# Optimization experiments

Measured on AMD Instinct MI355X. Metric: run time of the kernel, lower is better.

The kernel has to match this reference:

```python
import jax, jax.numpy as jnp
import numpy as np

NUM_HEADS = 32
NUM_KV_HEADS = 8
HEAD_DIM = 128
HIDDEN = 4096
BASE = 10000.0


def setup_inputs() -> dict:
    key = jax.random.key(0)
    ks = jax.random.split(key, 9)
    bs, seq = 1, 2048
    x = jax.random.normal(ks[0], (bs, seq, HIDDEN), dtype=jnp.float32)
    position_ids = jnp.broadcast_to(jnp.arange(seq, dtype=jnp.int32), (bs, seq))
    s = 1.0 / np.sqrt(HIDDEN)
    wq = jax.random.normal(ks[1], (NUM_HEADS * HEAD_DIM, HIDDEN), dtype=jnp.float32) * s
    bq = jnp.zeros((NUM_HEADS * HEAD_DIM,), dtype=jnp.float32)
    wk = jax.random.normal(ks[2], (NUM_KV_HEADS * HEAD_DIM, HIDDEN), dtype=jnp.float32) * s
    bk = jnp.zeros((NUM_KV_HEADS * HEAD_DIM,), dtype=jnp.float32)
    wv = jax.random.normal(ks[3], (NUM_KV_HEADS * HEAD_DIM, HIDDEN), dtype=jnp.float32) * s
    bv = jnp.zeros((NUM_KV_HEADS * HEAD_DIM,), dtype=jnp.float32)
    wo = jax.random.normal(ks[4], (HIDDEN, NUM_HEADS * HEAD_DIM), dtype=jnp.float32) * s
    bo = jnp.zeros((HIDDEN,), dtype=jnp.float32)
    return {"x": x, "position_ids": position_ids, "wq": wq, "bq": bq,
            "wk": wk, "bk": bk, "wv": wv, "bv": bv, "wo": wo, "bo": bo}


def _rotate_half(t):
    h = t.shape[-1] // 2
    return jnp.concatenate([-t[..., h:], t[..., :h]], axis=-1)


def _rope_cos_sin(position_ids, dtype):
    # inv_freq: (head_dim/2,)
    inv_freq = 1.0 / (BASE ** (jnp.arange(0, HEAD_DIM, 2, dtype=jnp.float32) / HEAD_DIM))
    freqs = position_ids.astype(jnp.float32)[..., None] * inv_freq  # (bs, seq, hd/2)
    emb = jnp.concatenate([freqs, freqs], axis=-1)  # (bs, seq, hd)
    return jnp.cos(emb).astype(dtype), jnp.sin(emb).astype(dtype)


def reference(x, position_ids, wq, bq, wk, bk, wv, bv, wo, bo):
    bs, seq, _ = x.shape
    g = NUM_HEADS // NUM_KV_HEADS
    # projections -> (bs, heads, seq, head_dim)
    q = (x @ wq.T + bq).reshape(bs, seq, NUM_HEADS, HEAD_DIM).transpose(0, 2, 1, 3)
    k = (x @ wk.T + bk).reshape(bs, seq, NUM_KV_HEADS, HEAD_DIM).transpose(0, 2, 1, 3)
    v = (x @ wv.T + bv).reshape(bs, seq, NUM_KV_HEADS, HEAD_DIM).transpose(0, 2, 1, 3)
    cos, sin = _rope_cos_sin(position_ids, x.dtype)
    cos, sin = cos[:, None], sin[:, None]  # broadcast over heads
    q = q * cos + _rotate_half(q) * sin
    k = k * cos + _rotate_half(k) * sin
    # grouped attention without expanding kv (same math as repeat_kv)
    qg = q.reshape(bs, NUM_KV_HEADS, g, seq, HEAD_DIM)
    scores = jnp.einsum('bhgqd,bhkd->bhgqk', qg, k) / jnp.sqrt(
        jnp.asarray(HEAD_DIM, dtype=jnp.float32)).astype(x.dtype)
    probs = jax.nn.softmax(scores.astype(jnp.float32), axis=-1).astype(x.dtype)
    out = jnp.einsum('bhgqk,bhkd->bhgqd', probs, v)  # (bs, kvh, g, seq, hd)
    out = out.reshape(bs, NUM_HEADS, seq, HEAD_DIM).transpose(0, 2, 1, 3)
    out = out.reshape(bs, seq, NUM_HEADS * HEAD_DIM)
    return out @ wo.T + bo
```

## Files before the change

kernel.cpp:

```cpp
#include <hip/hip_runtime.h>
#include <stdint.h>

typedef unsigned short u16;
typedef unsigned long long u64;
typedef __attribute__((ext_vector_type(8))) short s8v;
typedef __attribute__((ext_vector_type(4))) float f4v;

#define MFMA(a, b, c) __builtin_amdgcn_mfma_f32_16x16x32_bf16((a), (b), (c), 0, 0, 0)

__device__ __forceinline__ u16 f2b(float f) {
  uint32_t x = __float_as_uint(f);
  x += 0x7fff + ((x >> 16) & 1);
  return (u16)(x >> 16);
}
__device__ __forceinline__ float b2f(u16 u) {
  return __uint_as_float(((uint32_t)u) << 16);
}

__device__ __forceinline__ void gll16(const void* g, void* l) {
  __builtin_amdgcn_global_load_lds((const __attribute__((address_space(1))) uint32_t*)g,
                                   (__attribute__((address_space(3))) uint32_t*)l, 16, 0, 0);
}
__device__ __forceinline__ void bar() { __builtin_amdgcn_s_barrier(); }

__global__ void cvt_kernel(const float* __restrict__ src, u16* __restrict__ dst, int n8) {
  int i = blockIdx.x * 256 + threadIdx.x;
  if (i >= n8) return;
  const float4* s = (const float4*)src;
  float4 f0 = s[2 * (size_t)i], f1 = s[2 * (size_t)i + 1];
  s8v o;
  o[0] = (short)f2b(f0.x); o[1] = (short)f2b(f0.y); o[2] = (short)f2b(f0.z); o[3] = (short)f2b(f0.w);
  o[4] = (short)f2b(f1.x); o[5] = (short)f2b(f1.y); o[6] = (short)f2b(f1.z); o[7] = (short)f2b(f1.w);
  *(s8v*)(dst + 8 * (size_t)i) = o;
}

template <int BM, int MODE>
__global__ __launch_bounds__(512, 2) void gemm8p(
    const u16* __restrict__ A, const u16* __restrict__ Bact,
    const float* __restrict__ bA, const float* __restrict__ bB, const float* __restrict__ bC,
    float* __restrict__ Cf, u16* __restrict__ Cq, u16* __restrict__ Ck, u16* __restrict__ Cv,
    int K) {
  extern __shared__ u16 smem[];
  constexpr int AO = BM * 64;
  constexpr int BE = 2 * BM * 64;
  constexpr int BO = BE + 16384;
  constexpr int MI = BM / 64;

  const int tid = threadIdx.x;
  const int l = tid & 63, wv = tid >> 6;
  const int wm = wv >> 2, wn = wv & 3;
  const int lr = l & 15, lg = l >> 4;
  const int swz = 16 * (lr & 7);
  const int wrow = wm * (BM / 2);

  const int nwg = gridDim.x;
  int bid = blockIdx.x;
  bid = (bid & 7) * (nwg >> 3) + (bid >> 3);
  const int NB = 8;
  const int m0 = (bid / NB) * BM, n0 = (bid % NB) * 256;

  const size_t K64 = (size_t)64 * K;

  const int sr = tid >> 3;
  const int sc = ((tid & 7) ^ (sr & 7)) * 8;
  const u16* gA = A + (size_t)(m0 + sr) * K + sc;
  const u16* gB = Bact + (size_t)(n0 + sr) * K + sc;

  auto STA = [&](int P, int h, int kt) {
    const u16* g = gA + (size_t)(h * (BM / 2)) * K + (size_t)kt * 64;
    u16* d = smem + (P ? AO : 0) + h * (BM / 2) * 64 + tid * 8;
    gll16(g, d);
    if constexpr (BM == 256) gll16(g + K64, d + 4096);
  };
  auto STB = [&](int P, int h, int kt) {
    const u16* g = gB + (size_t)(h * 128) * K + (size_t)kt * 64;
    u16* d = smem + (P ? BO : BE) + h * 8192 + tid * 8;
    gll16(g, d);
    gll16(g + K64, d + 4096);
  };

  const char* smc = (const char*)smem;
  s8v a[MI][2], b0[2][2], b1[2][2];
  auto LDA = [&](int P, int QR) {
#pragma unroll
    for (int mi = 0; mi < MI; ++mi)
#pragma unroll
      for (int kk = 0; kk < 2; ++kk)
        a[mi][kk] = *(const s8v*)(smc + (P ? AO * 2 : 0) +
            (wrow + QR * (BM / 4) + mi * 16 + lr) * 128 + ((kk * 64 + lg * 16) ^ swz));
  };
  auto LDB = [&](int P, int QC, s8v bb[2][2]) {
#pragma unroll
    for (int ni = 0; ni < 2; ++ni)
#pragma unroll
      for (int kk = 0; kk < 2; ++kk)
        bb[ni][kk] = *(const s8v*)(smc + (P ? BO * 2 : BE * 2) +
            (wn * 64 + QC * 32 + ni * 16 + lr) * 128 + ((kk * 64 + lg * 16) ^ swz));
  };

  f4v acc[BM / 32][4];
#pragma unroll
  for (int i = 0; i < BM / 32; ++i)
#pragma unroll
    for (int j = 0; j < 4; ++j) acc[i][j] = {0.f, 0.f, 0.f, 0.f};

#define PHMF(QR, QC, B)                                                        \
  __builtin_amdgcn_s_setprio(1);                                               \
  _Pragma("unroll") for (int mi = 0; mi < MI; ++mi)                            \
    _Pragma("unroll") for (int ni = 0; ni < 2; ++ni)                           \
      _Pragma("unroll") for (int kk = 0; kk < 2; ++kk)                         \
        acc[(QR) * MI + mi][(QC) * 2 + ni] =                                   \
            MFMA(a[mi][kk], B[ni][kk], acc[(QR) * MI + mi][(QC) * 2 + ni]);    \
  __builtin_amdgcn_s_setprio(0);

  STB(0, 0, 0); STB(0, 1, 0);
  STA(0, 0, 0); STA(0, 1, 0);
  STB(1, 0, 1); STB(1, 1, 1);
  asm volatile("s_waitcnt vmcnt(4)" ::: "memory");
  bar();

  const int ITERS = K >> 7;
  for (int i = 0; i < ITERS; ++i) {
    const int kn = 2 * i + 2;
    const bool more = (i + 1 < ITERS);
    LDA(0, 0); LDB(0, 0, b0);
    STA(1, 0, 2 * i + 1);
    bar(); PHMF(0, 0, b0); bar();
    LDB(0, 1, b1);
    STA(1, 1, 2 * i + 1);
    bar(); PHMF(0, 1, b1); bar();
    LDA(0, 1);
    if (more) STB(0, 0, kn);
    bar(); PHMF(1, 1, b1); bar();
    if (more) STB(0, 1, kn);
    bar(); PHMF(1, 0, b0);
    asm volatile("s_waitcnt vmcnt(4)" ::: "memory");
    bar();
    LDA(1, 0); LDB(1, 0, b0);
    if (more) STA(0, 0, kn);
    bar(); PHMF(0, 0, b0); bar();
    LDB(1, 1, b1);
    if (more) STA(0, 1, kn);
    bar(); PHMF(0, 1, b1); bar();
    LDA(1, 1);
    if (more) STB(1, 0, 2 * i + 3);
    bar(); PHMF(1, 1, b1); bar();
    if (more) STB(1, 1, 2 * i + 3);
    bar(); PHMF(1, 0, b0);
    asm volatile("s_waitcnt vmcnt(4)" ::: "memory");
    bar();
  }
#undef PHMF

  bar();

  if (MODE == 2) {
    const int mt = m0 >> 8;
    if (mt < 20) {
      u16* dst; int fstride, fbase; const float* bias;
      if (mt < 16) { dst = Cq; fstride = 4096; fbase = m0;        bias = bA; }
      else         { dst = Ck; fstride = 1024; fbase = m0 - 4096; bias = bB; }
      u16* buf = smem + wv * 4352;
#pragma unroll
      for (int c = 0; c < 2; ++c) {
#pragma unroll
        for (int fj2 = 0; fj2 < 2; ++fj2) {
          const int fj = 2 * c + fj2;
          const int tl = fj2 * 16 + lr;
#pragma unroll
          for (int fi = 0; fi < BM / 32; ++fi)
#pragma unroll
            for (int r = 0; r < 4; ++r) {
              const int fl = fi * 16 + lg * 4 + r;
              buf[tl * 136 + fl] = f2b(acc[fi][fj][r] + bias[fbase + wrow + fl]);
            }
        }
        asm volatile("s_waitcnt lgkmcnt(0)" ::: "memory");
        const int row = l >> 1, half = l & 1;
        const int tok = n0 + wn * 64 + c * 32 + row;
        const u16* src = buf + row * 136 + half * 64;
        u16* g = dst + (size_t)tok * fstride + fbase + wrow + half * 64;
#pragma unroll
        for (int i = 0; i < 8; ++i)
          *(s8v*)(g + i * 8) = *(const s8v*)(src + i * 8);
        asm volatile("s_waitcnt lgkmcnt(0)" ::: "memory");
      }
    } else {
#pragma unroll
      for (int fi = 0; fi < BM / 32; ++fi)
#pragma unroll
        for (int fj = 0; fj < 4; ++fj)
#pragma unroll
          for (int r = 0; r < 4; ++r) {
            const int feat = m0 - 5120 + wrow + fi * 16 + lg * 4 + r;
            const int tok = n0 + wn * 64 + fj * 16 + lr;
            Cv[(size_t)feat * 2048 + tok] = f2b(acc[fi][fj][r] + bC[feat]);
          }
    }
  } else {
    float* buf = (float*)smem + wv * 1088;
#pragma unroll
    for (int c = 0; c < 4; ++c) {
#pragma unroll
      for (int fi = 0; fi < BM / 32; ++fi)
#pragma unroll
        for (int r = 0; r < 4; ++r) {
          const int fl = fi * 16 + lg * 4 + r;
          buf[lr * 68 + fl] = acc[fi][c][r] + bA[m0 + wrow + fl];
        }
      asm volatile("s_waitcnt lgkmcnt(0)" ::: "memory");
      const int row = l >> 2, q4 = l & 3;
      const int tok = n0 + wn * 64 + c * 16 + row;
      float* g = Cf + (size_t)tok * 4096 + m0 + wrow + q4 * 16;
      const float* src = buf + row * 68 + q4 * 16;
#pragma unroll
      for (int i = 0; i < 4; ++i)
        *(f4v*)(g + i * 4) = *(const f4v*)(src + i * 4);
      asm volatile("s_waitcnt lgkmcnt(0)" ::: "memory");
    }
  }
}

__global__ void rope_kernel(u16* __restrict__ q, u16* __restrict__ k, const int* __restrict__ pos) {
  int i = blockIdx.x * 256 + threadIdx.x;
  const int NQ = 2048 * 32 * 64;
  const int NK = 2048 * 8 * 64;
  u16* buf;
  int m, d, stride, h;
  if (i < NQ) { buf = q; m = i >> 11; h = (i >> 6) & 31; d = i & 63; stride = 4096; }
  else {
    i -= NQ; if (i >= NK) return;
    buf = k; m = i >> 9; h = (i >> 6) & 7; d = i & 63; stride = 1024;
  }
  size_t base = (size_t)m * stride + h * 128 + d;
  float a = b2f(buf[base]), b = b2f(buf[base + 64]);
  float p = (float)pos[m];
  float ang = p * exp2f(-0.20762050593045952f * (float)d);
  float s, c;
  sincosf(ang, &s, &c);
  buf[base]      = f2b(a * c - b * s);
  buf[base + 64] = f2b(b * c + a * s);
}

__global__ __launch_bounds__(512, 4) void attn_kernel(const u16* __restrict__ Q, const u16* __restrict__ Kb,
                                                      const u16* __restrict__ Vt, u16* __restrict__ Ao) {
  __shared__ __align__(16) u16 Ks[64 * 128];
  __shared__ __align__(16) u16 Vs[128 * 64];
  __shared__ __align__(16) u16 Ps[8 * 16 * 64];
  const int tid = threadIdx.x;
  const int l = tid & 63, wv = tid >> 6;
  const int lr = l & 15, lg = l >> 4;
  const int head = blockIdx.x >> 4, qt = blockIdx.x & 15;
  const int kh = head >> 2;
  const int qrow = qt * 128 + wv * 16 + lr;

  s8v qf[4];
#pragma unroll
  for (int s = 0; s < 4; ++s)
    qf[s] = *(const s8v*)&Q[(size_t)qrow * 4096 + head * 128 + s * 32 + lg * 8];

  f4v zero = {0.f, 0.f, 0.f, 0.f};
  f4v ao[8];
#pragma unroll
  for (int tt = 0; tt < 8; ++tt) ao[tt] = zero;
  float mrun = -1e30f, lrun = 0.f;

  const int ki0 = tid, ki1 = tid + 512;
  const int kr0 = ki0 >> 4, kc0 = (ki0 & 15) ^ (kr0 & 7);
  const int kr1 = ki1 >> 4, kc1 = (ki1 & 15) ^ (kr1 & 7);
  const int vr0 = ki0 >> 3, vc0 = (ki0 & 7) ^ (vr0 & 7);
  const int vr1 = ki1 >> 3, vc1 = (ki1 & 7) ^ (vr1 & 7);
  const u16* Kg = Kb + kh * 128;
  const u16* Vg = Vt + (size_t)(kh * 128) * 2048;
  const u16* kp0 = Kg + (size_t)kr0 * 1024 + kc0 * 8;
  const u16* kp1 = Kg + (size_t)kr1 * 1024 + kc1 * 8;
  const u16* vp0 = Vg + (size_t)vr0 * 2048 + vc0 * 8;
  const u16* vp1 = Vg + (size_t)vr1 * 2048 + vc1 * 8;

  char* KsB = (char*)Ks;
  char* VsB = (char*)Vs;
  char* PwB = (char*)Ps + wv * 2048;
  const int swz = 16 * (lr & 7);
  const float C2 = 0.12753102f;

  for (int t = 0; t < 2048; t += 64) {
    __syncthreads();
    gll16(kp0 + (size_t)t * 1024, KsB + ki0 * 16);
    gll16(kp1 + (size_t)t * 1024, KsB + ki1 * 16);
    gll16(vp0 + t,                VsB + ki0 * 16);
    gll16(vp1 + t,                VsB + ki1 * 16);
    __syncthreads();

    f4v c[4];
#pragma unroll
    for (int j = 0; j < 4; ++j) c[j] = zero;
#pragma unroll
    for (int s = 0; s < 4; ++s) {
#pragma unroll
      for (int j = 0; j < 4; ++j) {
        s8v kf = *(const s8v*)(KsB + (16 * j + lr) * 256 + (((4 * s + lg) * 16) ^ swz));
        c[j] = MFMA(kf, qf[s], c[j]);
      }
    }

    float mx = fmaxf(fmaxf(c[0][0], c[0][1]), fmaxf(c[0][2], c[0][3]));
#pragma unroll
    for (int j = 1; j < 4; ++j)
      mx = fmaxf(mx, fmaxf(fmaxf(c[j][0], c[j][1]), fmaxf(c[j][2], c[j][3])));
    mx = fmaxf(mx, __shfl_xor(mx, 16));
    mx = fmaxf(mx, __shfl_xor(mx, 32));
    float m2x = mx * C2;

    if (!__all(m2x - mrun <= 8.f)) {
      float mnew = fmaxf(mrun, m2x);
      float alpha = __builtin_amdgcn_exp2f(mrun - mnew);
      float ar[4];
#pragma unroll
      for (int r = 0; r < 4; ++r) ar[r] = __shfl(alpha, 4 * lg + r);
#pragma unroll
      for (int tt = 0; tt < 8; ++tt)
#pragma unroll
        for (int r = 0; r < 4; ++r) ao[tt][r] *= ar[r];
      lrun *= alpha;
      mrun = mnew;
    }

    float rs = 0.f;
#pragma unroll
    for (int j = 0; j < 4; ++j) {
      float p0 = __builtin_amdgcn_exp2f(__builtin_fmaf(c[j][0], C2, -mrun));
      float p1 = __builtin_amdgcn_exp2f(__builtin_fmaf(c[j][1], C2, -mrun));
      float p2 = __builtin_amdgcn_exp2f(__builtin_fmaf(c[j][2], C2, -mrun));
      float p3 = __builtin_amdgcn_exp2f(__builtin_fmaf(c[j][3], C2, -mrun));
      rs += (p0 + p1) + (p2 + p3);
      uint32_t lo = (uint32_t)f2b(p0) | ((uint32_t)f2b(p1) << 16);
      uint32_t hi = (uint32_t)f2b(p2) | ((uint32_t)f2b(p3) << 16);
      u64 pak = (u64)lo | ((u64)hi << 32);
      *(u64*)(PwB + lr * 128 + ((32 * j + 8 * lg) ^ swz)) = pak;
    }
    rs += __shfl_xor(rs, 16);
    rs += __shfl_xor(rs, 32);
    lrun += rs;

#pragma unroll
    for (int h = 0; h < 2; ++h) {
      s8v pf = *(const s8v*)(PwB + lr * 128 + ((64 * h + 16 * lg) ^ swz));
#pragma unroll
      for (int tt = 0; tt < 8; ++tt) {
        s8v vf = *(const s8v*)(VsB + (16 * tt + lr) * 128 + (((4 * h + lg) * 16) ^ swz));
        ao[tt] = MFMA(pf, vf, ao[tt]);
      }
    }
  }

  float inv = 1.f / lrun;
  float ir[4];
#pragma unroll
  for (int r = 0; r < 4; ++r) ir[r] = __shfl(inv, 4 * lg + r);
#pragma unroll
  for (int tt = 0; tt < 8; ++tt)
#pragma unroll
    for (int r = 0; r < 4; ++r)
      Ao[(size_t)(qt * 128 + wv * 16 + 4 * lg + r) * 4096 + head * 128 + 16 * tt + lr] =
          f2b(ao[tt][r] * ir[r]);
}

extern "C" void kernel_launch(void* const* d_in, const int* in_sizes, int n_in,
                              void* d_out, int out_size, void* d_ws, size_t ws_size,
                              hipStream_t stream) {
  const float* x  = (const float*)d_in[0];
  const int*   pos = (const int*)d_in[1];
  const float* wq = (const float*)d_in[2];
  const float* bq = (const float*)d_in[3];
  const float* wk = (const float*)d_in[4];
  const float* bk = (const float*)d_in[5];
  const float* wv = (const float*)d_in[6];
  const float* bv = (const float*)d_in[7];
  const float* wo = (const float*)d_in[8];
  const float* bo = (const float*)d_in[9];
  float* out = (float*)d_out;

  char* ws = (char*)d_ws;
  u16* xb   = (u16*)(ws + 0);
  u16* wqkv = (u16*)(ws + 16777216);
  u16* wob  = (u16*)(ws + 67108864);
  u16* qb   = (u16*)(ws + 100663296);
  u16* kb   = (u16*)(ws + 117440512);
  u16* vT   = (u16*)(ws + 121634816);
  u16* ab   = (u16*)(ws + 125829120);

  auto cv = [&](const float* s, u16* d, size_t n) {
    int n8 = (int)(n / 8);
    cvt_kernel<<<(n8 + 255) / 256, 256, 0, stream>>>(s, d, n8);
  };
  cv(x,  xb,   (size_t)2048 * 4096);
  cv(wq, wqkv, (size_t)4096 * 4096);
  cv(wk, wqkv + (size_t)4096 * 4096, (size_t)1024 * 4096);
  cv(wv, wqkv + (size_t)5120 * 4096, (size_t)1024 * 4096);
  cv(wo, wob,  (size_t)4096 * 4096);

  gemm8p<256, 2><<<192, 512, 131072, stream>>>(wqkv, xb, bq, bk, bv,
                                               nullptr, qb, kb, vT, 4096);
  rope_kernel<<<(2048 * 32 * 64 + 2048 * 8 * 64) / 256, 256, 0, stream>>>(qb, kb, pos);
  attn_kernel<<<512, 512, 0, stream>>>(qb, kb, vT, ab);
  gemm8p<128, 0><<<256, 512, 98304, stream>>>(wob, ab, bo, nullptr, nullptr,
                                              out, nullptr, nullptr, nullptr, 4096);
}
```

Before: 347.0 us.

## Use 192-row QKV GEMM tiles, merge conversion kernels, concatenate biases

Changes the fused QKV projection GEMM from 256-row to 192-row tiles so 6144 rows give 256 workgroups instead of 192, which fits the CU count better. The A-tile staging loop and the epilogue are generalized so one tile can straddle the Q/K/V boundaries, with a per-fragment split between direct V writes and LDS-staged Q/K writes. The five fp32-to-bf16 conversion launches are merged into one kernel, and the biases are copied into one contiguous buffer with three async device copies. The cost is more complex epilogue branching and extra small memcpy launches.

```diff
diff --git a/kernel.cpp b/kernel.cpp
--- a/kernel.cpp
+++ b/kernel.cpp
@@ -23,21 +23,29 @@
 }
 __device__ __forceinline__ void bar() { __builtin_amdgcn_s_barrier(); }
 
-__global__ void cvt_kernel(const float* __restrict__ src, u16* __restrict__ dst, int n8) {
+__global__ void cvt_all(const float* __restrict__ x, const float* __restrict__ wq,
+                        const float* __restrict__ wk, const float* __restrict__ wv,
+                        const float* __restrict__ wo,
+                        u16* __restrict__ xb, u16* __restrict__ wqkv, u16* __restrict__ wob) {
   int i = blockIdx.x * 256 + threadIdx.x;
-  if (i >= n8) return;
-  const float4* s = (const float4*)src;
-  float4 f0 = s[2 * (size_t)i], f1 = s[2 * (size_t)i + 1];
+  const float* s; u16* d; size_t off;
+  if      (i < 1048576) { s = x;  d = xb;   off = (size_t)i; }
+  else if (i < 3145728) { s = wq; d = wqkv; off = (size_t)(i - 1048576); }
+  else if (i < 3670016) { s = wk; d = wqkv + (size_t)16777216; off = (size_t)(i - 3145728); }
+  else if (i < 4194304) { s = wv; d = wqkv + (size_t)20971520; off = (size_t)(i - 3670016); }
+  else                  { s = wo; d = wob;  off = (size_t)(i - 4194304); }
+  const float4* sp = (const float4*)(s + off * 8);
+  float4 f0 = sp[0], f1 = sp[1];
   s8v o;
   o[0] = (short)f2b(f0.x); o[1] = (short)f2b(f0.y); o[2] = (short)f2b(f0.z); o[3] = (short)f2b(f0.w);
   o[4] = (short)f2b(f1.x); o[5] = (short)f2b(f1.y); o[6] = (short)f2b(f1.z); o[7] = (short)f2b(f1.w);
-  *(s8v*)(dst + 8 * (size_t)i) = o;
+  *(s8v*)(d + off * 8) = o;
 }
 
 template <int BM, int MODE>
 __global__ __launch_bounds__(512, 2) void gemm8p(
     const u16* __restrict__ A, const u16* __restrict__ Bact,
-    const float* __restrict__ bA, const float* __restrict__ bB, const float* __restrict__ bC,
+    const float* __restrict__ bias,
     float* __restrict__ Cf, u16* __restrict__ Cq, u16* __restrict__ Ck, u16* __restrict__ Cv,
     int K) {
   extern __shared__ u16 smem[];
@@ -45,6 +53,7 @@
   constexpr int BE = 2 * BM * 64;
   constexpr int BO = BE + 16384;
   constexpr int MI = BM / 64;
+  constexpr int NH = BM / 64;
 
   const int tid = threadIdx.x;
   const int l = tid & 63, wv = tid >> 6;
@@ -67,10 +76,8 @@
   const u16* gB = Bact + (size_t)(n0 + sr) * K + sc;
 
   auto STA = [&](int P, int h, int kt) {
-    const u16* g = gA + (size_t)(h * (BM / 2)) * K + (size_t)kt * 64;
-    u16* d = smem + (P ? AO : 0) + h * (BM / 2) * 64 + tid * 8;
-    gll16(g, d);
-    if constexpr (BM == 256) gll16(g + K64, d + 4096);
+    gll16(gA + (size_t)(h * 64) * K + (size_t)kt * 64,
+          smem + (P ? AO : 0) + h * 4096 + tid * 8);
   };
   auto STB = [&](int P, int h, int kt) {
     const u16* g = gB + (size_t)(h * 128) * K + (size_t)kt * 64;
@@ -114,7 +121,8 @@
   __builtin_amdgcn_s_setprio(0);
 
   STB(0, 0, 0); STB(0, 1, 0);
-  STA(0, 0, 0); STA(0, 1, 0);
+#pragma unroll
+  for (int h = 0; h < NH; ++h) STA(0, h, 0);
   STB(1, 0, 1); STB(1, 1, 1);
   asm volatile("s_waitcnt vmcnt(4)" ::: "memory");
   bar();
@@ -130,11 +138,13 @@
     STA(1, 1, 2 * i + 1);
     bar(); PHMF(0, 1, b1); bar();
     LDA(0, 1);
+    if constexpr (NH > 2) STA(1, 2, 2 * i + 1);
     if (more) STB(0, 0, kn);
     bar(); PHMF(1, 1, b1); bar();
     if (more) STB(0, 1, kn);
     bar(); PHMF(1, 0, b0);
-    asm volatile("s_waitcnt vmcnt(4)" ::: "memory");
+    if (more) asm volatile("s_waitcnt vmcnt(4)" ::: "memory");
+    else      asm volatile("s_waitcnt vmcnt(0)" ::: "memory");
     bar();
     LDA(1, 0); LDB(1, 0, b0);
     if (more) STA(0, 0, kn);
@@ -143,7 +153,10 @@
     if (more) STA(0, 1, kn);
     bar(); PHMF(0, 1, b1); bar();
     LDA(1, 1);
-    if (more) STB(1, 0, 2 * i + 3);
+    if (more) {
+      if constexpr (NH > 2) STA(0, 2, kn);
+      STB(1, 0, 2 * i + 3);
+    }
     bar(); PHMF(1, 1, b1); bar();
     if (more) STB(1, 1, 2 * i + 3);
     bar(); PHMF(1, 0, b0);
@@ -154,13 +167,23 @@
 
   bar();
 
-  if (MODE == 2) {
-    const int mt = m0 >> 8;
-    if (mt < 20) {
-      u16* dst; int fstride, fbase; const float* bias;
-      if (mt < 16) { dst = Cq; fstride = 4096; fbase = m0;        bias = bA; }
-      else         { dst = Ck; fstride = 1024; fbase = m0 - 4096; bias = bB; }
-      u16* buf = smem + wv * 4352;
+  if constexpr (MODE == 2) {
+#pragma unroll
+    for (int fi = 0; fi < BM / 32; ++fi) {
+      const int f0 = m0 + wrow + fi * 16;
+      if (f0 >= 5120) {
+#pragma unroll
+        for (int fj = 0; fj < 4; ++fj)
+#pragma unroll
+          for (int r = 0; r < 4; ++r) {
+            const int f = f0 + lg * 4 + r;
+            const int tok = n0 + wn * 64 + fj * 16 + lr;
+            Cv[(size_t)(f - 5120) * 2048 + tok] = f2b(acc[fi][fj][r] + bias[f]);
+          }
+      }
+    }
+    if (m0 + wrow < 5120) {
+      u16* buf = smem + wv * 3328;
 #pragma unroll
       for (int c = 0; c < 2; ++c) {
 #pragma unroll
@@ -168,34 +191,31 @@
           const int fj = 2 * c + fj2;
           const int tl = fj2 * 16 + lr;
 #pragma unroll
-          for (int fi = 0; fi < BM / 32; ++fi)
-#pragma unroll
-            for (int r = 0; r < 4; ++r) {
-              const int fl = fi * 16 + lg * 4 + r;
-              buf[tl * 136 + fl] = f2b(acc[fi][fj][r] + bias[fbase + wrow + fl]);
+          for (int fi = 0; fi < BM / 32; ++fi) {
+            const int f0 = m0 + wrow + fi * 16;
+            if (f0 < 5120) {
+#pragma unroll
+              for (int r = 0; r < 4; ++r) {
+                const int fl = fi * 16 + lg * 4 + r;
+                buf[tl * 104 + fl] = f2b(acc[fi][fj][r] + bias[m0 + wrow + fl]);
+              }
             }
+          }
         }
         asm volatile("s_waitcnt lgkmcnt(0)" ::: "memory");
         const int row = l >> 1, half = l & 1;
         const int tok = n0 + wn * 64 + c * 32 + row;
-        const u16* src = buf + row * 136 + half * 64;
-        u16* g = dst + (size_t)tok * fstride + fbase + wrow + half * 64;
-#pragma unroll
-        for (int i = 0; i < 8; ++i)
-          *(s8v*)(g + i * 8) = *(const s8v*)(src + i * 8);
+#pragma unroll
+        for (int i2 = 0; i2 < 6; ++i2) {
+          const int flc = (2 * i2 + half) * 8;
+          const int f = m0 + wrow + flc;
+          if (f < 4096)
+            *(s8v*)(Cq + (size_t)tok * 4096 + f) = *(const s8v*)(buf + row * 104 + flc);
+          else if (f < 5120)
+            *(s8v*)(Ck + (size_t)tok * 1024 + (f - 4096)) = *(const s8v*)(buf + row * 104 + flc);
+        }
         asm volatile("s_waitcnt lgkmcnt(0)" ::: "memory");
       }
-    } else {
-#pragma unroll
-      for (int fi = 0; fi < BM / 32; ++fi)
-#pragma unroll
-        for (int fj = 0; fj < 4; ++fj)
-#pragma unroll
-          for (int r = 0; r < 4; ++r) {
-            const int feat = m0 - 5120 + wrow + fi * 16 + lg * 4 + r;
-            const int tok = n0 + wn * 64 + fj * 16 + lr;
-            Cv[(size_t)feat * 2048 + tok] = f2b(acc[fi][fj][r] + bC[feat]);
-          }
     }
   } else {
     float* buf = (float*)smem + wv * 1088;
@@ -206,7 +226,7 @@
 #pragma unroll
         for (int r = 0; r < 4; ++r) {
           const int fl = fi * 16 + lg * 4 + r;
-          buf[lr * 68 + fl] = acc[fi][c][r] + bA[m0 + wrow + fl];
+          buf[lr * 68 + fl] = acc[fi][c][r] + bias[m0 + wrow + fl];
         }
       asm volatile("s_waitcnt lgkmcnt(0)" ::: "memory");
       const int row = l >> 2, q4 = l & 3;
@@ -214,8 +234,8 @@
       float* g = Cf + (size_t)tok * 4096 + m0 + wrow + q4 * 16;
       const float* src = buf + row * 68 + q4 * 16;
 #pragma unroll
-      for (int i = 0; i < 4; ++i)
-        *(f4v*)(g + i * 4) = *(const f4v*)(src + i * 4);
+      for (int i2 = 0; i2 < 4; ++i2)
+        *(f4v*)(g + i2 * 4) = *(const f4v*)(src + i2 * 4);
       asm volatile("s_waitcnt lgkmcnt(0)" ::: "memory");
     }
   }
@@ -388,21 +408,18 @@
   u16* kb   = (u16*)(ws + 117440512);
   u16* vT   = (u16*)(ws + 121634816);
   u16* ab   = (u16*)(ws + 125829120);
-
-  auto cv = [&](const float* s, u16* d, size_t n) {
-    int n8 = (int)(n / 8);
-    cvt_kernel<<<(n8 + 255) / 256, 256, 0, stream>>>(s, d, n8);
-  };
-  cv(x,  xb,   (size_t)2048 * 4096);
-  cv(wq, wqkv, (size_t)4096 * 4096);
-  cv(wk, wqkv + (size_t)4096 * 4096, (size_t)1024 * 4096);
-  cv(wv, wqkv + (size_t)5120 * 4096, (size_t)1024 * 4096);
-  cv(wo, wob,  (size_t)4096 * 4096);
-
-  gemm8p<256, 2><<<192, 512, 131072, stream>>>(wqkv, xb, bq, bk, bv,
+  float* bqkv = (float*)(ws + 142606336);
+
+  hipMemcpyAsync(bqkv,        bq, 4096 * sizeof(float), hipMemcpyDeviceToDevice, stream);
+  hipMemcpyAsync(bqkv + 4096, bk, 1024 * sizeof(float), hipMemcpyDeviceToDevice, stream);
+  hipMemcpyAsync(bqkv + 5120, bv, 1024 * sizeof(float), hipMemcpyDeviceToDevice, stream);
+
+  cvt_all<<<24576, 256, 0, stream>>>(x, wq, wk, wv, wo, xb, wqkv, wob);
+
+  gemm8p<192, 2><<<256, 512, 114688, stream>>>(wqkv, xb, bqkv,
                                                nullptr, qb, kb, vT, 4096);
   rope_kernel<<<(2048 * 32 * 64 + 2048 * 8 * 64) / 256, 256, 0, stream>>>(qb, kb, pos);
   attn_kernel<<<512, 512, 0, stream>>>(qb, kb, vT, ab);
-  gemm8p<128, 0><<<256, 512, 98304, stream>>>(wob, ab, bo, nullptr, nullptr,
+  gemm8p<128, 0><<<256, 512, 98304, stream>>>(wob, ab, bo,
                                               out, nullptr, nullptr, nullptr, 4096);
 }
```

After: 326.1 us. 1.06x faster.
